# Performance work log

Measured on AMD Instinct MI355X. Metric: run time of the kernel, lower is better.

Reference implementation:

```python
import jax, jax.numpy as jnp
import numpy as np
from functools import partial

B, T, F, H = 32768, 48, 16, 32  # batch, horizon, feature dim, rnn_size


def setup_inputs() -> dict:
    key = jax.random.key(0)
    ks = jax.random.split(key, 9)
    return {
        "decoder_feature": jax.random.normal(ks[0], (B, T, F), dtype=jnp.float32),
        "decoder_init_input": jax.random.normal(ks[1], (B, 1), dtype=jnp.float32),
        "init_state": jax.random.normal(ks[2], (B, H), dtype=jnp.float32),
        # GRUCell (Keras default reset_after=True): kernel [in_dim, 3H], recurrent [H, 3H], two biases
        "kernel": jax.random.normal(ks[3], (1 + F, 3 * H), dtype=jnp.float32) * 0.1,
        "recurrent_kernel": jax.random.normal(ks[4], (H, 3 * H), dtype=jnp.float32) * 0.1,
        "bias_x": jax.random.normal(ks[5], (3 * H,), dtype=jnp.float32) * 0.1,
        "bias_h": jax.random.normal(ks[6], (3 * H,), dtype=jnp.float32) * 0.1,
        "dense_w": jax.random.normal(ks[7], (H, 1), dtype=jnp.float32) * 0.1,
        "dense_b": jax.random.normal(ks[8], (1,), dtype=jnp.float32) * 0.1,
    }


def reference(decoder_feature, decoder_init_input, init_state,
              kernel, recurrent_kernel, bias_x, bias_h, dense_w, dense_b):
    units = init_state.shape[-1]

    def step(carry, feat_t):
        h, prev_out = carry                              # h: [B,H], prev_out: [B,1]
        x = jnp.concatenate([prev_out, feat_t], axis=1)  # [B, 1+F]
        mx = x @ kernel + bias_x                         # [B, 3H]
        mh = h @ recurrent_kernel + bias_h               # [B, 3H] (reset_after=True)
        xz, xr, xh = jnp.split(mx, 3, axis=1)
        hz, hr, hh_in = jnp.split(mh, 3, axis=1)
        z = jax.nn.sigmoid(xz + hz)
        r = jax.nn.sigmoid(xr + hr)
        hh = jnp.tanh(xh + r * hh_in)
        h_new = z * h + (1.0 - z) * hh                   # GRU output == new state
        out = h_new @ dense_w + dense_b                  # Dense(1): [B,1]
        return (h_new, out), out

    feats = jnp.transpose(decoder_feature, (1, 0, 2))    # [T,B,F] time-major for scan
    _, outs = jax.lax.scan(step, (init_state, decoder_init_input), feats)
    return jnp.transpose(outs, (1, 0, 2))                # [B,T,1]
```

## Files before the change

kernel.cpp:

```cpp
#include <hip/hip_runtime.h>


typedef __attribute__((ext_vector_type(8))) short short8;
typedef __attribute__((ext_vector_type(4))) float f32x4;

constexpr int T_STEPS  = 48;
constexpr int F_DIM    = 16;
constexpr int H_DIM    = 32;
constexpr int O_STRIDE = 17;

union S8 { short8 s; unsigned u[4]; };

__device__ __forceinline__ unsigned pk_bf16(float hi, float lo) {
    return __builtin_amdgcn_perm(__float_as_uint(hi) + 0x8000u,
                                 __float_as_uint(lo) + 0x8000u, 0x07060302u);
}
__device__ __forceinline__ short bf16s(float x) {
    return (short)((__float_as_uint(x) + 0x8000u) >> 16);
}
__device__ __forceinline__ float rcpf(float x) { return __builtin_amdgcn_rcpf(x); }
__device__ __forceinline__ float ex2(float x)  { return __builtin_amdgcn_exp2f(x); }
#define MFMA(a, b, c) __builtin_amdgcn_mfma_f32_16x16x32_bf16(a, b, c, 0, 0, 0)
#define SWZ16(v) __int_as_float(__builtin_amdgcn_ds_swizzle(__float_as_int(v), 0x401F))
#define BPERM(a, v) __builtin_amdgcn_ds_bpermute((a), (v))

__global__ __launch_bounds__(64, 2)
void gru_mfma11(const float* __restrict__ feat,
                const float* __restrict__ init_in,
                const float* __restrict__ init_h,
                const float* __restrict__ Wk,
                const float* __restrict__ Rk,
                const float* __restrict__ bx,
                const float* __restrict__ bh,
                const float* __restrict__ dw,
                const float* __restrict__ db,
                float* __restrict__ out)
{
    __shared__ __align__(16) float obuf[T_STEPS * O_STRIDE];

    const int lane = threadIdx.x;
    const int ln   = lane & 15;
    const int quad = lane >> 4;
    const int b0   = blockIdx.x * 16;
    const int bpa  = (lane ^ 32) << 2;

    const float SZ = -1.44269504088896340736f;
    const float SC =  2.88539008177792681472f;

    const int cA0 = (ln >> 2) * 8 + (ln & 3);
    const int cA1 = cA0 + 4;

    S8 WzA, WrA, WhA, WzB, WrB, WhB, RzA, RrA, RhA, RzB, RrB, RhB;
#pragma unroll
    for (int j = 0; j < 8; ++j) {
        const int k = quad * 8 + j;
        float wzA = 0, wrA = 0, whA = 0, wzB = 0, wrB = 0, whB = 0;
        if (k < 16) {
            const float* Wrow = Wk + (size_t)(k + 1) * 96;
            wzA = Wrow[cA0]; wrA = Wrow[32 + cA0]; whA = Wrow[64 + cA0];
            wzB = Wrow[cA1]; wrB = Wrow[32 + cA1]; whB = Wrow[64 + cA1];
        } else if (k < 18) {
            wzA = Wk[cA0]; wrA = Wk[32 + cA0]; whA = Wk[64 + cA0];
            wzB = Wk[cA1]; wrB = Wk[32 + cA1]; whB = Wk[64 + cA1];
        }
        WzA.s[j] = bf16s(SZ * wzA); WrA.s[j] = bf16s(SZ * wrA); WhA.s[j] = bf16s(SC * whA);
        WzB.s[j] = bf16s(SZ * wzB); WrB.s[j] = bf16s(SZ * wrB); WhB.s[j] = bf16s(SC * whB);
        const float* Rrow = Rk + (size_t)k * 96;
        RzA.s[j] = bf16s(SZ * Rrow[cA0]); RrA.s[j] = bf16s(SZ * Rrow[32 + cA0]);
        RhA.s[j] = bf16s(SC * Rrow[64 + cA0]);
        RzB.s[j] = bf16s(SZ * Rrow[cA1]); RrB.s[j] = bf16s(SZ * Rrow[32 + cA1]);
        RhB.s[j] = bf16s(SC * Rrow[64 + cA1]);
    }

    f32x4 czA, crA, chA, cgA, czB, crB, chB, cgB, dwA, dwB;
#pragma unroll
    for (int i = 0; i < 4; ++i) {
        const int c0 = quad * 8 + i, c1 = c0 + 4;
        czA[i] = SZ * (bx[c0] + bh[c0]);           czB[i] = SZ * (bx[c1] + bh[c1]);
        crA[i] = SZ * (bx[32 + c0] + bh[32 + c0]); crB[i] = SZ * (bx[32 + c1] + bh[32 + c1]);
        chA[i] = SC * bx[64 + c0];                 chB[i] = SC * bx[64 + c1];
        cgA[i] = SC * bh[64 + c0];                 cgB[i] = SC * bh[64 + c1];
        dwA[i] = dw[c0];                           dwB[i] = dw[c1];
    }
    const float dbs = db[0];

    f32x4 hcA, hcB;
#pragma unroll
    for (int i = 0; i < 4; ++i) {
        hcA[i] = init_h[(size_t)(b0 + ln) * H_DIM + quad * 8 + i];
        hcB[i] = init_h[(size_t)(b0 + ln) * H_DIM + quad * 8 + 4 + i];
    }
    S8 hB;
    hB.u[0] = pk_bf16(hcA[1], hcA[0]);
    hB.u[1] = pk_bf16(hcA[3], hcA[2]);
    hB.u[2] = pk_bf16(hcB[1], hcB[0]);
    hB.u[3] = pk_bf16(hcB[3], hcB[2]);

    float po = init_in[b0 + ln];

    const float* fqb = feat + (size_t)(b0 + ln) * (T_STEPS * F_DIM) + (quad & 1) * 8;
    f32x4 pa0 = *(const f32x4*)(fqb);
    f32x4 pb0 = *(const f32x4*)(fqb + 4);
    f32x4 pa1 = *(const f32x4*)(fqb + F_DIM);
    f32x4 pb1 = *(const f32x4*)(fqb + F_DIM + 4);

#define GRU_STEP(T_, PA_, PB_) do {                                            \
        S8 xa;                                                                 \
        {                                                                      \
            const unsigned zm = (quad < 2) ? 0xFFFFFFFFu : 0u;                 \
            xa.u[0] = pk_bf16(PA_[1], PA_[0]) & zm;                            \
            xa.u[1] = pk_bf16(PA_[3], PA_[2]) & zm;                            \
            xa.u[2] = pk_bf16(PB_[1], PB_[0]) & zm;                            \
            xa.u[3] = pk_bf16(PB_[3], PB_[2]) & zm;                            \
            if (quad == 2) {            \
                const float ph = __uint_as_float(                              \
                    (__float_as_uint(po) + 0x8000u) & 0xFFFF0000u);            \
                xa.u[0] = pk_bf16(po - ph, ph);                                \
            }                                                                  \
        }                                                                      \
        {                                             \
            const int t2 = ((T_) + 2 < T_STEPS) ? (T_) + 2 : T_STEPS - 1;      \
            PA_ = *(const f32x4*)(fqb + t2 * F_DIM);                           \
            PB_ = *(const f32x4*)(fqb + t2 * F_DIM + 4);                       \
        }                                                                      \
                                              \
        f32x4 aZA = czA, aRA = crA, aHA = chA, aGA = cgA;                      \
        f32x4 aZB = czB, aRB = crB, aHB = chB, aGB = cgB;                      \
        aZA = MFMA(WzA.s, xa.s, aZA);  aZB = MFMA(WzB.s, xa.s, aZB);           \
        aRA = MFMA(WrA.s, xa.s, aRA);  aRB = MFMA(WrB.s, xa.s, aRB);           \
        aHA = MFMA(WhA.s, xa.s, aHA);  aHB = MFMA(WhB.s, xa.s, aHB);           \
        aZA = MFMA(RzA.s, hB.s, aZA);  aZB = MFMA(RzB.s, hB.s, aZB);           \
        aRA = MFMA(RrA.s, hB.s, aRA);  aRB = MFMA(RrB.s, hB.s, aRB);           \
        aGA = MFMA(RhA.s, hB.s, aGA);  aGB = MFMA(RhB.s, hB.s, aGB);           \
                                   \
        _Pragma("unroll")                                                      \
        for (int i = 0; i < 4; ++i) {                                          \
            {                                                                  \
                const float Ez = ex2(aZA[i]);                                  \
                const float rr = rcpf(1.0f + ex2(aRA[i]));                     \
                const float vv = fmaf(rr, aGA[i], aHA[i]);                     \
                const float Dv = 1.0f + ex2(vv);                               \
                const float num = fmaf(hcA[i], Dv, (Dv - 2.0f) * Ez);          \
                const float den = fmaf(Dv, Ez, Dv);                            \
                hcA[i] = num * rcpf(den);                                      \
            }                                                                  \
            {                                                                  \
                const float Ez = ex2(aZB[i]);                                  \
                const float rr = rcpf(1.0f + ex2(aRB[i]));                     \
                const float vv = fmaf(rr, aGB[i], aHB[i]);                     \
                const float Dv = 1.0f + ex2(vv);                               \
                const float num = fmaf(hcB[i], Dv, (Dv - 2.0f) * Ez);          \
                const float den = fmaf(Dv, Ez, Dv);                            \
                hcB[i] = num * rcpf(den);                                      \
            }                                                                  \
        }                                                                      \
                   \
        hB.u[0] = pk_bf16(hcA[1], hcA[0]);                                     \
        hB.u[1] = pk_bf16(hcA[3], hcA[2]);                                     \
        hB.u[2] = pk_bf16(hcB[1], hcB[0]);                                     \
        hB.u[3] = pk_bf16(hcB[3], hcB[2]);                                     \
                   \
        float s = fmaf(hcA[0], dwA[0], hcA[1] * dwA[1]);                       \
        s = fmaf(hcA[2], dwA[2], s);                                           \
        s = fmaf(hcA[3], dwA[3], s);                                           \
        s = fmaf(hcB[0], dwB[0], s);                                           \
        s = fmaf(hcB[1], dwB[1], s);                                           \
        s = fmaf(hcB[2], dwB[2], s);                                           \
        s = fmaf(hcB[3], dwB[3], s);                                           \
        s += SWZ16(s);                                                         \
        s += __int_as_float(BPERM(bpa, __float_as_int(s)));                    \
        po = s + dbs;                                                          \
        if (lane < 16) obuf[(T_) * O_STRIDE + lane] = po;                      \
    } while (0)

    for (int t = 0; t < T_STEPS; t += 2) {
        GRU_STEP(t,     pa0, pb0);
        GRU_STEP(t + 1, pa1, pb1);
    }
#undef GRU_STEP

    __builtin_amdgcn_s_waitcnt(0xC07F);
    {
        const int row = lane >> 2;
        const int tb  = (lane & 3) * 12;
        float* orow = out + (size_t)(b0 + row) * T_STEPS + tb;
#pragma unroll
        for (int k = 0; k < 3; ++k) {
            f32x4 v;
#pragma unroll
            for (int e = 0; e < 4; ++e) v[e] = obuf[(tb + k * 4 + e) * O_STRIDE + row];
            *(f32x4*)(orow + k * 4) = v;
        }
    }
}

extern "C" void kernel_launch(void* const* d_in, const int* in_sizes, int n_in,
                              void* d_out, int out_size, void* d_ws, size_t ws_size,
                              hipStream_t stream) {
    const float* feat    = (const float*)d_in[0];
    const float* init_in = (const float*)d_in[1];
    const float* init_h  = (const float*)d_in[2];
    const float* Wk      = (const float*)d_in[3];
    const float* Rk      = (const float*)d_in[4];
    const float* bx      = (const float*)d_in[5];
    const float* bh      = (const float*)d_in[6];
    const float* dw      = (const float*)d_in[7];
    const float* db      = (const float*)d_in[8];
    float* out           = (float*)d_out;

    const int B = in_sizes[2] / H_DIM;
    dim3 grid((unsigned)(B / 16));
    dim3 block(64);
    hipLaunchKernelGGL(gru_mfma11, grid, block, 0, stream,
                       feat, init_in, init_h, Wk, Rk, bx, bh, dw, db, out);
}
```

Baseline: 173.1 us.

## Interleave two independent batch tiles per wave to hide recurrence latency

Each 64-lane wave now processes two 16-row batch tiles, interleaving their MFMA, gate math and output reductions in one step so the two dependency chains overlap within the wave. Grid size is halved and launch bounds relaxed to occupancy 1 to allow the larger register footprint. The per-wave weight setup is amortized over twice the rows. The risk is that fewer resident waves per SIMD remove the inter-wave latency hiding that the old layout already had.

```diff
diff --git a/kernel.cpp b/kernel.cpp
--- a/kernel.cpp
+++ b/kernel.cpp
@@ -24,8 +24,8 @@
 #define SWZ16(v) __int_as_float(__builtin_amdgcn_ds_swizzle(__float_as_int(v), 0x401F))
 #define BPERM(a, v) __builtin_amdgcn_ds_bpermute((a), (v))
 
-__global__ __launch_bounds__(64, 2)
-void gru_mfma11(const float* __restrict__ feat,
+__global__ __launch_bounds__(64, 1)
+void gru_mfma12(const float* __restrict__ feat,
                 const float* __restrict__ init_in,
                 const float* __restrict__ init_h,
                 const float* __restrict__ Wk,
@@ -36,12 +36,12 @@
                 const float* __restrict__ db,
                 float* __restrict__ out)
 {
-    __shared__ __align__(16) float obuf[T_STEPS * O_STRIDE];
+    __shared__ __align__(16) float obuf[2 * T_STEPS * O_STRIDE];
 
     const int lane = threadIdx.x;
     const int ln   = lane & 15;
     const int quad = lane >> 4;
-    const int b0   = blockIdx.x * 16;
+    const int b0   = blockIdx.x * 32;
     const int bpa  = (lane ^ 32) << 2;
 
     const float SZ = -1.44269504088896340736f;
@@ -84,112 +84,169 @@
     }
     const float dbs = db[0];
 
-    f32x4 hcA, hcB;
+    f32x4 hcA0, hcB0, hcA1, hcB1;
 #pragma unroll
     for (int i = 0; i < 4; ++i) {
-        hcA[i] = init_h[(size_t)(b0 + ln) * H_DIM + quad * 8 + i];
-        hcB[i] = init_h[(size_t)(b0 + ln) * H_DIM + quad * 8 + 4 + i];
-    }
-    S8 hB;
-    hB.u[0] = pk_bf16(hcA[1], hcA[0]);
-    hB.u[1] = pk_bf16(hcA[3], hcA[2]);
-    hB.u[2] = pk_bf16(hcB[1], hcB[0]);
-    hB.u[3] = pk_bf16(hcB[3], hcB[2]);
-
-    float po = init_in[b0 + ln];
-
-    const float* fqb = feat + (size_t)(b0 + ln) * (T_STEPS * F_DIM) + (quad & 1) * 8;
-    f32x4 pa0 = *(const f32x4*)(fqb);
-    f32x4 pb0 = *(const f32x4*)(fqb + 4);
-    f32x4 pa1 = *(const f32x4*)(fqb + F_DIM);
-    f32x4 pb1 = *(const f32x4*)(fqb + F_DIM + 4);
-
-#define GRU_STEP(T_, PA_, PB_) do {                                            \
-        S8 xa;                                                                 \
+        hcA0[i] = init_h[(size_t)(b0 + ln) * H_DIM + quad * 8 + i];
+        hcB0[i] = init_h[(size_t)(b0 + ln) * H_DIM + quad * 8 + 4 + i];
+        hcA1[i] = init_h[(size_t)(b0 + 16 + ln) * H_DIM + quad * 8 + i];
+        hcB1[i] = init_h[(size_t)(b0 + 16 + ln) * H_DIM + quad * 8 + 4 + i];
+    }
+    S8 hB0, hB1;
+    hB0.u[0] = pk_bf16(hcA0[1], hcA0[0]); hB0.u[1] = pk_bf16(hcA0[3], hcA0[2]);
+    hB0.u[2] = pk_bf16(hcB0[1], hcB0[0]); hB0.u[3] = pk_bf16(hcB0[3], hcB0[2]);
+    hB1.u[0] = pk_bf16(hcA1[1], hcA1[0]); hB1.u[1] = pk_bf16(hcA1[3], hcA1[2]);
+    hB1.u[2] = pk_bf16(hcB1[1], hcB1[0]); hB1.u[3] = pk_bf16(hcB1[3], hcB1[2]);
+
+    float po0 = init_in[b0 + ln];
+    float po1 = init_in[b0 + 16 + ln];
+
+    const float* fq0 = feat + (size_t)(b0 + ln) * (T_STEPS * F_DIM) + (quad & 1) * 8;
+    const float* fq1 = feat + (size_t)(b0 + 16 + ln) * (T_STEPS * F_DIM) + (quad & 1) * 8;
+    f32x4 p0a0 = *(const f32x4*)(fq0);
+    f32x4 p0b0 = *(const f32x4*)(fq0 + 4);
+    f32x4 p0a1 = *(const f32x4*)(fq0 + F_DIM);
+    f32x4 p0b1 = *(const f32x4*)(fq0 + F_DIM + 4);
+    f32x4 p1a0 = *(const f32x4*)(fq1);
+    f32x4 p1b0 = *(const f32x4*)(fq1 + 4);
+    f32x4 p1a1 = *(const f32x4*)(fq1 + F_DIM);
+    f32x4 p1b1 = *(const f32x4*)(fq1 + F_DIM + 4);
+
+#define STEP2(T_, PA0_, PB0_, PA1_, PB1_) do {                                 \
+        S8 xa0, xa1;                                                           \
         {                                                                      \
             const unsigned zm = (quad < 2) ? 0xFFFFFFFFu : 0u;                 \
-            xa.u[0] = pk_bf16(PA_[1], PA_[0]) & zm;                            \
-            xa.u[1] = pk_bf16(PA_[3], PA_[2]) & zm;                            \
-            xa.u[2] = pk_bf16(PB_[1], PB_[0]) & zm;                            \
-            xa.u[3] = pk_bf16(PB_[3], PB_[2]) & zm;                            \
+            xa0.u[0] = pk_bf16(PA0_[1], PA0_[0]) & zm;                         \
+            xa0.u[1] = pk_bf16(PA0_[3], PA0_[2]) & zm;                         \
+            xa0.u[2] = pk_bf16(PB0_[1], PB0_[0]) & zm;                         \
+            xa0.u[3] = pk_bf16(PB0_[3], PB0_[2]) & zm;                         \
+            xa1.u[0] = pk_bf16(PA1_[1], PA1_[0]) & zm;                         \
+            xa1.u[1] = pk_bf16(PA1_[3], PA1_[2]) & zm;                         \
+            xa1.u[2] = pk_bf16(PB1_[1], PB1_[0]) & zm;                         \
+            xa1.u[3] = pk_bf16(PB1_[3], PB1_[2]) & zm;                         \
             if (quad == 2) {            \
-                const float ph = __uint_as_float(                              \
-                    (__float_as_uint(po) + 0x8000u) & 0xFFFF0000u);            \
-                xa.u[0] = pk_bf16(po - ph, ph);                                \
-            }                                                                  \
-        }                                                                      \
-        {                                             \
+                const float ph0 = __uint_as_float(                             \
+                    (__float_as_uint(po0) + 0x8000u) & 0xFFFF0000u);           \
+                const float ph1 = __uint_as_float(                             \
+                    (__float_as_uint(po1) + 0x8000u) & 0xFFFF0000u);           \
+                xa0.u[0] = pk_bf16(po0 - ph0, ph0);                            \
+                xa1.u[0] = pk_bf16(po1 - ph1, ph1);                            \
+            }                                                                  \
+        }                                                                      \
+        {                                 \
             const int t2 = ((T_) + 2 < T_STEPS) ? (T_) + 2 : T_STEPS - 1;      \
-            PA_ = *(const f32x4*)(fqb + t2 * F_DIM);                           \
-            PB_ = *(const f32x4*)(fqb + t2 * F_DIM + 4);                       \
-        }                                                                      \
-                                              \
-        f32x4 aZA = czA, aRA = crA, aHA = chA, aGA = cgA;                      \
-        f32x4 aZB = czB, aRB = crB, aHB = chB, aGB = cgB;                      \
-        aZA = MFMA(WzA.s, xa.s, aZA);  aZB = MFMA(WzB.s, xa.s, aZB);           \
-        aRA = MFMA(WrA.s, xa.s, aRA);  aRB = MFMA(WrB.s, xa.s, aRB);           \
-        aHA = MFMA(WhA.s, xa.s, aHA);  aHB = MFMA(WhB.s, xa.s, aHB);           \
-        aZA = MFMA(RzA.s, hB.s, aZA);  aZB = MFMA(RzB.s, hB.s, aZB);           \
-        aRA = MFMA(RrA.s, hB.s, aRA);  aRB = MFMA(RrB.s, hB.s, aRB);           \
-        aGA = MFMA(RhA.s, hB.s, aGA);  aGB = MFMA(RhB.s, hB.s, aGB);           \
-                                   \
+            PA0_ = *(const f32x4*)(fq0 + t2 * F_DIM);                          \
+            PB0_ = *(const f32x4*)(fq0 + t2 * F_DIM + 4);                      \
+            PA1_ = *(const f32x4*)(fq1 + t2 * F_DIM);                          \
+            PB1_ = *(const f32x4*)(fq1 + t2 * F_DIM + 4);                      \
+        }                                                                      \
+                \
+        f32x4 aZA0 = czA, aRA0 = crA, aHA0 = chA, aGA0 = cgA;                  \
+        f32x4 aZB0 = czB, aRB0 = crB, aHB0 = chB, aGB0 = cgB;                  \
+        f32x4 aZA1 = czA, aRA1 = crA, aHA1 = chA, aGA1 = cgA;                  \
+        f32x4 aZB1 = czB, aRB1 = crB, aHB1 = chB, aGB1 = cgB;                  \
+        aZA0 = MFMA(WzA.s, xa0.s, aZA0);  aZA1 = MFMA(WzA.s, xa1.s, aZA1);     \
+        aZB0 = MFMA(WzB.s, xa0.s, aZB0);  aZB1 = MFMA(WzB.s, xa1.s, aZB1);     \
+        aRA0 = MFMA(WrA.s, xa0.s, aRA0);  aRA1 = MFMA(WrA.s, xa1.s, aRA1);     \
+        aRB0 = MFMA(WrB.s, xa0.s, aRB0);  aRB1 = MFMA(WrB.s, xa1.s, aRB1);     \
+        aHA0 = MFMA(WhA.s, xa0.s, aHA0);  aHA1 = MFMA(WhA.s, xa1.s, aHA1);     \
+        aHB0 = MFMA(WhB.s, xa0.s, aHB0);  aHB1 = MFMA(WhB.s, xa1.s, aHB1);     \
+        aZA0 = MFMA(RzA.s, hB0.s, aZA0);  aZA1 = MFMA(RzA.s, hB1.s, aZA1);     \
+        aZB0 = MFMA(RzB.s, hB0.s, aZB0);  aZB1 = MFMA(RzB.s, hB1.s, aZB1);     \
+        aRA0 = MFMA(RrA.s, hB0.s, aRA0);  aRA1 = MFMA(RrA.s, hB1.s, aRA1);     \
+        aRB0 = MFMA(RrB.s, hB0.s, aRB0);  aRB1 = MFMA(RrB.s, hB1.s, aRB1);     \
+        aGA0 = MFMA(RhA.s, hB0.s, aGA0);  aGA1 = MFMA(RhA.s, hB1.s, aGA1);     \
+        aGB0 = MFMA(RhB.s, hB0.s, aGB0);  aGB1 = MFMA(RhB.s, hB1.s, aGB1);     \
+                  \
         _Pragma("unroll")                                                      \
         for (int i = 0; i < 4; ++i) {                                          \
             {                                                                  \
-                const float Ez = ex2(aZA[i]);                                  \
-                const float rr = rcpf(1.0f + ex2(aRA[i]));                     \
-                const float vv = fmaf(rr, aGA[i], aHA[i]);                     \
-                const float Dv = 1.0f + ex2(vv);                               \
-                const float num = fmaf(hcA[i], Dv, (Dv - 2.0f) * Ez);          \
-                const float den = fmaf(Dv, Ez, Dv);                            \
-                hcA[i] = num * rcpf(den);                                      \
-            }                                                                  \
-            {                                                                  \
-                const float Ez = ex2(aZB[i]);                                  \
-                const float rr = rcpf(1.0f + ex2(aRB[i]));                     \
-                const float vv = fmaf(rr, aGB[i], aHB[i]);                     \
-                const float Dv = 1.0f + ex2(vv);                               \
-                const float num = fmaf(hcB[i], Dv, (Dv - 2.0f) * Ez);          \
-                const float den = fmaf(Dv, Ez, Dv);                            \
-                hcB[i] = num * rcpf(den);                                      \
-            }                                                                  \
-        }                                                                      \
-                   \
-        hB.u[0] = pk_bf16(hcA[1], hcA[0]);                                     \
-        hB.u[1] = pk_bf16(hcA[3], hcA[2]);                                     \
-        hB.u[2] = pk_bf16(hcB[1], hcB[0]);                                     \
-        hB.u[3] = pk_bf16(hcB[3], hcB[2]);                                     \
-                   \
-        float s = fmaf(hcA[0], dwA[0], hcA[1] * dwA[1]);                       \
-        s = fmaf(hcA[2], dwA[2], s);                                           \
-        s = fmaf(hcA[3], dwA[3], s);                                           \
-        s = fmaf(hcB[0], dwB[0], s);                                           \
-        s = fmaf(hcB[1], dwB[1], s);                                           \
-        s = fmaf(hcB[2], dwB[2], s);                                           \
-        s = fmaf(hcB[3], dwB[3], s);                                           \
-        s += SWZ16(s);                                                         \
-        s += __int_as_float(BPERM(bpa, __float_as_int(s)));                    \
-        po = s + dbs;                                                          \
-        if (lane < 16) obuf[(T_) * O_STRIDE + lane] = po;                      \
+                const float Ez = ex2(aZA0[i]);                                 \
+                const float rr = rcpf(1.0f + ex2(aRA0[i]));                    \
+                const float vv = fmaf(rr, aGA0[i], aHA0[i]);                   \
+                const float Dv = 1.0f + ex2(vv);                               \
+                const float num = fmaf(hcA0[i], Dv, (Dv - 2.0f) * Ez);         \
+                const float den = fmaf(Dv, Ez, Dv);                            \
+                hcA0[i] = num * rcpf(den);                                     \
+            }                                                                  \
+            {                                                                  \
+                const float Ez = ex2(aZA1[i]);                                 \
+                const float rr = rcpf(1.0f + ex2(aRA1[i]));                    \
+                const float vv = fmaf(rr, aGA1[i], aHA1[i]);                   \
+                const float Dv = 1.0f + ex2(vv);                               \
+                const float num = fmaf(hcA1[i], Dv, (Dv - 2.0f) * Ez);         \
+                const float den = fmaf(Dv, Ez, Dv);                            \
+                hcA1[i] = num * rcpf(den);                                     \
+            }                                                                  \
+            {                                                                  \
+                const float Ez = ex2(aZB0[i]);                                 \
+                const float rr = rcpf(1.0f + ex2(aRB0[i]));                    \
+                const float vv = fmaf(rr, aGB0[i], aHB0[i]);                   \
+                const float Dv = 1.0f + ex2(vv);                               \
+                const float num = fmaf(hcB0[i], Dv, (Dv - 2.0f) * Ez);         \
+                const float den = fmaf(Dv, Ez, Dv);                            \
+                hcB0[i] = num * rcpf(den);                                     \
+            }                                                                  \
+            {                                                                  \
+                const float Ez = ex2(aZB1[i]);                                 \
+                const float rr = rcpf(1.0f + ex2(aRB1[i]));                    \
+                const float vv = fmaf(rr, aGB1[i], aHB1[i]);                   \
+                const float Dv = 1.0f + ex2(vv);                               \
+                const float num = fmaf(hcB1[i], Dv, (Dv - 2.0f) * Ez);         \
+                const float den = fmaf(Dv, Ez, Dv);                            \
+                hcB1[i] = num * rcpf(den);                                     \
+            }                                                                  \
+        }                                                                      \
+                                \
+        hB0.u[0] = pk_bf16(hcA0[1], hcA0[0]);                                  \
+        hB0.u[1] = pk_bf16(hcA0[3], hcA0[2]);                                  \
+        hB0.u[2] = pk_bf16(hcB0[1], hcB0[0]);                                  \
+        hB0.u[3] = pk_bf16(hcB0[3], hcB0[2]);                                  \
+        hB1.u[0] = pk_bf16(hcA1[1], hcA1[0]);                                  \
+        hB1.u[1] = pk_bf16(hcA1[3], hcA1[2]);                                  \
+        hB1.u[2] = pk_bf16(hcB1[1], hcB1[0]);                                  \
+        hB1.u[3] = pk_bf16(hcB1[3], hcB1[2]);                                  \
+                  \
+        float s0 = fmaf(hcA0[0], dwA[0], hcA0[1] * dwA[1])                     \
+                 + fmaf(hcA0[2], dwA[2], hcA0[3] * dwA[3]);                    \
+        float u0 = fmaf(hcB0[0], dwB[0], hcB0[1] * dwB[1])                     \
+                 + fmaf(hcB0[2], dwB[2], hcB0[3] * dwB[3]);                    \
+        float s1 = fmaf(hcA1[0], dwA[0], hcA1[1] * dwA[1])                     \
+                 + fmaf(hcA1[2], dwA[2], hcA1[3] * dwA[3]);                    \
+        float u1 = fmaf(hcB1[0], dwB[0], hcB1[1] * dwB[1])                     \
+                 + fmaf(hcB1[2], dwB[2], hcB1[3] * dwB[3]);                    \
+        s0 += u0; s1 += u1;                                                    \
+        s0 += SWZ16(s0); s1 += SWZ16(s1);                                      \
+        s0 += __int_as_float(BPERM(bpa, __float_as_int(s0)));                  \
+        s1 += __int_as_float(BPERM(bpa, __float_as_int(s1)));                  \
+        po0 = s0 + dbs; po1 = s1 + dbs;                                        \
+        if (lane < 16) {                                                       \
+            obuf[(T_) * O_STRIDE + lane] = po0;                                \
+            obuf[T_STEPS * O_STRIDE + (T_) * O_STRIDE + lane] = po1;           \
+        }                                                                      \
     } while (0)
 
     for (int t = 0; t < T_STEPS; t += 2) {
-        GRU_STEP(t,     pa0, pb0);
-        GRU_STEP(t + 1, pa1, pb1);
-    }
-#undef GRU_STEP
+        STEP2(t,     p0a0, p0b0, p1a0, p1b0);
+        STEP2(t + 1, p0a1, p0b1, p1a1, p1b1);
+    }
+#undef STEP2
 
     __builtin_amdgcn_s_waitcnt(0xC07F);
     {
         const int row = lane >> 2;
         const int tb  = (lane & 3) * 12;
-        float* orow = out + (size_t)(b0 + row) * T_STEPS + tb;
-#pragma unroll
-        for (int k = 0; k < 3; ++k) {
-            f32x4 v;
-#pragma unroll
-            for (int e = 0; e < 4; ++e) v[e] = obuf[(tb + k * 4 + e) * O_STRIDE + row];
-            *(f32x4*)(orow + k * 4) = v;
+#pragma unroll
+        for (int tile = 0; tile < 2; ++tile) {
+            const float* ob = obuf + tile * (T_STEPS * O_STRIDE);
+            float* orow = out + (size_t)(b0 + tile * 16 + row) * T_STEPS + tb;
+#pragma unroll
+            for (int k = 0; k < 3; ++k) {
+                f32x4 v;
+#pragma unroll
+                for (int e = 0; e < 4; ++e) v[e] = ob[(tb + k * 4 + e) * O_STRIDE + row];
+                *(f32x4*)(orow + k * 4) = v;
+            }
         }
     }
 }
@@ -209,8 +266,8 @@
     float* out           = (float*)d_out;
 
     const int B = in_sizes[2] / H_DIM;
-    dim3 grid((unsigned)(B / 16));
+    dim3 grid((unsigned)(B / 32));
     dim3 block(64);
-    hipLaunchKernelGGL(gru_mfma11, grid, block, 0, stream,
+    hipLaunchKernelGGL(gru_mfma12, grid, block, 0, stream,
                        feat, init_in, init_h, Wk, Rk, bx, bh, dw, db, out);
 }
```

After: 182.8 us. 5.6% more time.

## Fold dense output feedback into recurrent weights to break serial dependency

Applied to the files above, without the earlier changes.

Folds the Dense(1) output feedback into the recurrent and bias terms algebraically: prev_out·W_row0 becomes h·(dw⊗W_row0) plus db·W_row0. The next step's input no longer waits on the cross-lane reduction of the previous output, which shortens the per-step critical path. A first-step correction value carries the difference between the given init input and the implied output. The cost is two extra MFMAs per step (the candidate-gate feedback cannot merge with the reset-scaled recurrent term) and some extra bf16 rounding error in the folded weights. The output reduction also uses a shallower summation tree.

```diff
diff --git a/kernel.cpp b/kernel.cpp
--- a/kernel.cpp
+++ b/kernel.cpp
@@ -25,7 +25,7 @@
 #define BPERM(a, v) __builtin_amdgcn_ds_bpermute((a), (v))
 
 __global__ __launch_bounds__(64, 2)
-void gru_mfma11(const float* __restrict__ feat,
+void gru_mfma13(const float* __restrict__ feat,
                 const float* __restrict__ init_in,
                 const float* __restrict__ init_h,
                 const float* __restrict__ Wk,
@@ -50,7 +50,7 @@
     const int cA0 = (ln >> 2) * 8 + (ln & 3);
     const int cA1 = cA0 + 4;
 
-    S8 WzA, WrA, WhA, WzB, WrB, WhB, RzA, RrA, RhA, RzB, RrB, RhB;
+    S8 WzA, WrA, WhA, WzB, WrB, WhB, RzA, RrA, RhA, RzB, RrB, RhB, DwhA, DwhB;
 #pragma unroll
     for (int j = 0; j < 8; ++j) {
         const int k = quad * 8 + j;
@@ -66,23 +66,33 @@
         WzA.s[j] = bf16s(SZ * wzA); WrA.s[j] = bf16s(SZ * wrA); WhA.s[j] = bf16s(SC * whA);
         WzB.s[j] = bf16s(SZ * wzB); WrB.s[j] = bf16s(SZ * wrB); WhB.s[j] = bf16s(SC * whB);
         const float* Rrow = Rk + (size_t)k * 96;
-        RzA.s[j] = bf16s(SZ * Rrow[cA0]); RrA.s[j] = bf16s(SZ * Rrow[32 + cA0]);
-        RhA.s[j] = bf16s(SC * Rrow[64 + cA0]);
-        RzB.s[j] = bf16s(SZ * Rrow[cA1]); RrB.s[j] = bf16s(SZ * Rrow[32 + cA1]);
-        RhB.s[j] = bf16s(SC * Rrow[64 + cA1]);
-    }
-
+        const float dwk = dw[k];
+        RzA.s[j]  = bf16s(SZ * (Rrow[cA0]      + dwk * Wk[cA0]));
+        RrA.s[j]  = bf16s(SZ * (Rrow[32 + cA0] + dwk * Wk[32 + cA0]));
+        RhA.s[j]  = bf16s(SC * Rrow[64 + cA0]);
+        DwhA.s[j] = bf16s(SC * dwk * Wk[64 + cA0]);
+        RzB.s[j]  = bf16s(SZ * (Rrow[cA1]      + dwk * Wk[cA1]));
+        RrB.s[j]  = bf16s(SZ * (Rrow[32 + cA1] + dwk * Wk[32 + cA1]));
+        RhB.s[j]  = bf16s(SC * Rrow[64 + cA1]);
+        DwhB.s[j] = bf16s(SC * dwk * Wk[64 + cA1]);
+    }
+
+    const float dbs = db[0];
     f32x4 czA, crA, chA, cgA, czB, crB, chB, cgB, dwA, dwB;
 #pragma unroll
     for (int i = 0; i < 4; ++i) {
         const int c0 = quad * 8 + i, c1 = c0 + 4;
-        czA[i] = SZ * (bx[c0] + bh[c0]);           czB[i] = SZ * (bx[c1] + bh[c1]);
-        crA[i] = SZ * (bx[32 + c0] + bh[32 + c0]); crB[i] = SZ * (bx[32 + c1] + bh[32 + c1]);
-        chA[i] = SC * bx[64 + c0];                 chB[i] = SC * bx[64 + c1];
-        cgA[i] = SC * bh[64 + c0];                 cgB[i] = SC * bh[64 + c1];
-        dwA[i] = dw[c0];                           dwB[i] = dw[c1];
-    }
-    const float dbs = db[0];
+        czA[i] = SZ * (bx[c0] + bh[c0] + dbs * Wk[c0]);
+        czB[i] = SZ * (bx[c1] + bh[c1] + dbs * Wk[c1]);
+        crA[i] = SZ * (bx[32 + c0] + bh[32 + c0] + dbs * Wk[32 + c0]);
+        crB[i] = SZ * (bx[32 + c1] + bh[32 + c1] + dbs * Wk[32 + c1]);
+        chA[i] = SC * (bx[64 + c0] + dbs * Wk[64 + c0]);
+        chB[i] = SC * (bx[64 + c1] + dbs * Wk[64 + c1]);
+        cgA[i] = SC * bh[64 + c0];
+        cgB[i] = SC * bh[64 + c1];
+        dwA[i] = dw[c0];
+        dwB[i] = dw[c1];
+    }
 
     f32x4 hcA, hcB;
 #pragma unroll
@@ -96,7 +106,16 @@
     hB.u[2] = pk_bf16(hcB[1], hcB[0]);
     hB.u[3] = pk_bf16(hcB[3], hcB[2]);
 
-    float po = init_in[b0 + ln];
+    float pv;
+    {
+        float d = fmaf(hcA[0], dwA[0], hcA[1] * dwA[1])
+                + fmaf(hcA[2], dwA[2], hcA[3] * dwA[3]);
+        d += fmaf(hcB[0], dwB[0], hcB[1] * dwB[1])
+           + fmaf(hcB[2], dwB[2], hcB[3] * dwB[3]);
+        d += SWZ16(d);
+        d += __int_as_float(BPERM(bpa, __float_as_int(d)));
+        pv = init_in[b0 + ln] - (d + dbs);
+    }
 
     const float* fqb = feat + (size_t)(b0 + ln) * (T_STEPS * F_DIM) + (quad & 1) * 8;
     f32x4 pa0 = *(const f32x4*)(fqb);
@@ -112,10 +131,10 @@
             xa.u[1] = pk_bf16(PA_[3], PA_[2]) & zm;                            \
             xa.u[2] = pk_bf16(PB_[1], PB_[0]) & zm;                            \
             xa.u[3] = pk_bf16(PB_[3], PB_[2]) & zm;                            \
-            if (quad == 2) {            \
+            if (quad == 2) {        \
                 const float ph = __uint_as_float(                              \
-                    (__float_as_uint(po) + 0x8000u) & 0xFFFF0000u);            \
-                xa.u[0] = pk_bf16(po - ph, ph);                                \
+                    (__float_as_uint(pv) + 0x8000u) & 0xFFFF0000u);            \
+                xa.u[0] = pk_bf16(pv - ph, ph);                                \
             }                                                                  \
         }                                                                      \
         {                                             \
@@ -123,16 +142,17 @@
             PA_ = *(const f32x4*)(fqb + t2 * F_DIM);                           \
             PB_ = *(const f32x4*)(fqb + t2 * F_DIM + 4);                       \
         }                                                                      \
-                                              \
+           \
         f32x4 aZA = czA, aRA = crA, aHA = chA, aGA = cgA;                      \
         f32x4 aZB = czB, aRB = crB, aHB = chB, aGB = cgB;                      \
-        aZA = MFMA(WzA.s, xa.s, aZA);  aZB = MFMA(WzB.s, xa.s, aZB);           \
-        aRA = MFMA(WrA.s, xa.s, aRA);  aRB = MFMA(WrB.s, xa.s, aRB);           \
-        aHA = MFMA(WhA.s, xa.s, aHA);  aHB = MFMA(WhB.s, xa.s, aHB);           \
-        aZA = MFMA(RzA.s, hB.s, aZA);  aZB = MFMA(RzB.s, hB.s, aZB);           \
-        aRA = MFMA(RrA.s, hB.s, aRA);  aRB = MFMA(RrB.s, hB.s, aRB);           \
-        aGA = MFMA(RhA.s, hB.s, aGA);  aGB = MFMA(RhB.s, hB.s, aGB);           \
-                                   \
+        aZA = MFMA(WzA.s, xa.s, aZA);   aZB = MFMA(WzB.s, xa.s, aZB);          \
+        aRA = MFMA(WrA.s, xa.s, aRA);   aRB = MFMA(WrB.s, xa.s, aRB);          \
+        aHA = MFMA(WhA.s, xa.s, aHA);   aHB = MFMA(WhB.s, xa.s, aHB);          \
+        aZA = MFMA(RzA.s, hB.s, aZA);   aZB = MFMA(RzB.s, hB.s, aZB);          \
+        aRA = MFMA(RrA.s, hB.s, aRA);   aRB = MFMA(RrB.s, hB.s, aRB);          \
+        aHA = MFMA(DwhA.s, hB.s, aHA);  aHB = MFMA(DwhB.s, hB.s, aHB);         \
+        aGA = MFMA(RhA.s, hB.s, aGA);   aGB = MFMA(RhB.s, hB.s, aGB);          \
+                 \
         _Pragma("unroll")                                                      \
         for (int i = 0; i < 4; ++i) {                                          \
             {                                                                  \
@@ -154,23 +174,20 @@
                 hcB[i] = num * rcpf(den);                                      \
             }                                                                  \
         }                                                                      \
-                   \
+           \
         hB.u[0] = pk_bf16(hcA[1], hcA[0]);                                     \
         hB.u[1] = pk_bf16(hcA[3], hcA[2]);                                     \
         hB.u[2] = pk_bf16(hcB[1], hcB[0]);                                     \
         hB.u[3] = pk_bf16(hcB[3], hcB[2]);                                     \
-                   \
-        float s = fmaf(hcA[0], dwA[0], hcA[1] * dwA[1]);                       \
-        s = fmaf(hcA[2], dwA[2], s);                                           \
-        s = fmaf(hcA[3], dwA[3], s);                                           \
-        s = fmaf(hcB[0], dwB[0], s);                                           \
-        s = fmaf(hcB[1], dwB[1], s);                                           \
-        s = fmaf(hcB[2], dwB[2], s);                                           \
-        s = fmaf(hcB[3], dwB[3], s);                                           \
+                \
+        float s = fmaf(hcA[0], dwA[0], hcA[1] * dwA[1])                        \
+                + fmaf(hcA[2], dwA[2], hcA[3] * dwA[3]);                       \
+        s += fmaf(hcB[0], dwB[0], hcB[1] * dwB[1])                             \
+           + fmaf(hcB[2], dwB[2], hcB[3] * dwB[3]);                            \
         s += SWZ16(s);                                                         \
         s += __int_as_float(BPERM(bpa, __float_as_int(s)));                    \
-        po = s + dbs;                                                          \
-        if (lane < 16) obuf[(T_) * O_STRIDE + lane] = po;                      \
+        if (lane < 16) obuf[(T_) * O_STRIDE + lane] = s + dbs;                 \
+        pv = 0.0f;                           \
     } while (0)
 
     for (int t = 0; t < T_STEPS; t += 2) {
@@ -211,6 +228,6 @@
     const int B = in_sizes[2] / H_DIM;
     dim3 grid((unsigned)(B / 16));
     dim3 block(64);
-    hipLaunchKernelGGL(gru_mfma11, grid, block, 0, stream,
+    hipLaunchKernelGGL(gru_mfma13, grid, block, 0, stream,
                        feat, init_in, init_h, Wk, Rk, bx, bh, dw, db, out);
 }
```

Measured after the change: 177.8 us. 1.03x slower.
